# Kernel optimization log

Measured on AMD Instinct MI355X. Metric: run time of the kernel, lower is better.

The kernel has to match this reference:

```python
import jax, jax.numpy as jnp
import numpy as np
import math

Z_DIM = 1024
DOWN = 512
UP = 1024
HEADS = 16
ROPE_HD = 64
HEAD_DIM = Z_DIM // HEADS  # 64, used only in softmax scale
V_HD = UP // HEADS


def _rope(x, num_heads, head_dim, base=10000.0):
    # x: [bs, L, num_heads*head_dim] -> [bs, num_heads, L, head_dim]
    bs, L, _ = x.shape
    theta = 1.0 / (base ** (jnp.arange(0, head_dim, 2, dtype=jnp.float32) / head_dim))
    pe = jnp.arange(L, dtype=jnp.float32)[:, None] * theta[None, :]  # [L, hd/2]
    # NOTE: faithful to source, which stores sin(pos) in cos_pos and cos(pos) in sin_pos
    cos_pos = jnp.repeat(jnp.sin(pe), 2, axis=-1)  # [L, hd]
    sin_pos = jnp.repeat(jnp.cos(pe), 2, axis=-1)
    q = x.reshape(bs, L, num_heads, head_dim).transpose(0, 2, 1, 3)
    q2 = jnp.stack([-q[..., 1::2], q[..., ::2]], axis=-1).reshape(q.shape)
    return q * cos_pos + q2 * sin_pos


def setup_inputs() -> dict:
    key = jax.random.key(0)
    ks = jax.random.split(key, 20)
    B, S = 2, 2048
    s = lambda fan_in: 1.0 / math.sqrt(fan_in)
    d = {
        'query': jax.random.normal(ks[0], (B, S, Z_DIM), jnp.float32),
        'key': jax.random.normal(ks[1], (B, S, Z_DIM), jnp.float32),
        'value': jax.random.normal(ks[2], (B, S, Z_DIM), jnp.float32),
        'w_dkv': jax.random.uniform(ks[3], (Z_DIM, DOWN), jnp.float32, -s(Z_DIM), s(Z_DIM)),
        'b_dkv': jnp.zeros((DOWN,), jnp.float32),
        'w_uk': jax.random.uniform(ks[4], (DOWN, UP), jnp.float32, -s(DOWN), s(DOWN)),
        'b_uk': jnp.zeros((UP,), jnp.float32),
        'w_uv': jax.random.uniform(ks[5], (DOWN, UP), jnp.float32, -s(DOWN), s(DOWN)),
        'b_uv': jnp.zeros((UP,), jnp.float32),
        'w_dq': jax.random.uniform(ks[6], (Z_DIM, DOWN), jnp.float32, -s(Z_DIM), s(Z_DIM)),
        'b_dq': jnp.zeros((DOWN,), jnp.float32),
        'w_uq': jax.random.uniform(ks[7], (DOWN, UP), jnp.float32, -s(DOWN), s(DOWN)),
        'b_uq': jnp.zeros((UP,), jnp.float32),
        'w_qr': jax.random.uniform(ks[8], (DOWN, ROPE_HD * HEADS), jnp.float32, -s(DOWN), s(DOWN)),
        'b_qr': jnp.zeros((ROPE_HD * HEADS,), jnp.float32),
        'w_kr': jax.random.uniform(ks[9], (Z_DIM, ROPE_HD), jnp.float32, -s(Z_DIM), s(Z_DIM)),
        'b_kr': jnp.zeros((ROPE_HD,), jnp.float32),
        'w_fc': jax.random.uniform(ks[10], (HEADS * V_HD, Z_DIM), jnp.float32, -s(HEADS * V_HD), s(HEADS * V_HD)),
        'b_fc': jnp.zeros((Z_DIM,), jnp.float32),
    }
    return d


def reference(query, key, value, w_dkv, b_dkv, w_uk, b_uk, w_uv, b_uv,
              w_dq, b_dq, w_uq, b_uq, w_qr, b_qr, w_kr, b_kr, w_fc, b_fc):
    bs, S, _ = query.shape
    c_t_kv = key @ w_dkv + b_dkv                      # [B,S,down]
    k_t_c = c_t_kv @ w_uk + b_uk                      # [B,S,up]
    v_t_c = c_t_kv @ w_uv + b_uv                      # [B,S,up]
    c_t_q = query @ w_dq + b_dq                       # [B,S,down]
    q_t_c = c_t_q @ w_uq + b_uq                       # [B,S,up]
    q_t_r = _rope(c_t_q @ w_qr + b_qr, HEADS, ROPE_HD)  # [B,H,S,rope_hd]
    k_t_r = _rope(key @ w_kr + b_kr, 1, ROPE_HD)         # [B,1,S,rope_hd]

    q_t_c = q_t_c.reshape(bs, S, HEADS, V_HD).transpose(0, 2, 1, 3)  # [B,H,S,dc]
    q = jnp.concatenate([q_t_c, q_t_r], axis=-1)                      # [B,H,S,dc+dr]
    k_t_c = k_t_c.reshape(bs, S, HEADS, V_HD).transpose(0, 2, 1, 3)
    k = jnp.concatenate([k_t_c, jnp.broadcast_to(k_t_r, (bs, HEADS, S, ROPE_HD))], axis=-1)

    scores = jnp.einsum('bhqd,bhkd->bhqk', q, k)
    scale = math.sqrt(HEAD_DIM) + math.sqrt(ROPE_HD)
    attn = jax.nn.softmax(scores / scale, axis=-1)    # dropout is identity (eval / p=0)

    v = v_t_c.reshape(bs, S, HEADS, V_HD).transpose(0, 2, 1, 3)
    out = jnp.einsum('bhqk,bhkd->bhqd', attn, v)      # [B,H,S,v_hd]
    out = out.transpose(0, 2, 1, 3).reshape(bs, S, HEADS * V_HD)
    return out @ w_fc + b_fc
```

## Files before the change

kernel.cpp:

```cpp
#include <hip/hip_runtime.h>
#include <hip/hip_bf16.h>
#include <hip/hip_fp16.h>

typedef __attribute__((ext_vector_type(8))) short    bf16x8;
typedef __attribute__((ext_vector_type(4))) float    f32x4;
typedef __attribute__((ext_vector_type(4))) _Float16 f16x4;
typedef __attribute__((ext_vector_type(8))) _Float16 f16x8;
typedef __attribute__((ext_vector_type(2))) __fp16   fp16x2_raw;

typedef const void __attribute__((address_space(1))) gvoid_t;
typedef void __attribute__((address_space(3)))       lvoid_t;

static __device__ __forceinline__ void gload_lds16(const void* g, void* l) {
    __builtin_amdgcn_global_load_lds((gvoid_t*)g, (lvoid_t*)l, 16, 0, 0);
}

static __device__ __forceinline__ short bfbits(float f) {
    union { __hip_bfloat16 h; short s; } u;
    u.h = __float2bfloat16(f);
    return u.s;
}

static __device__ __forceinline__ float rope_val(float val, int col, int row, int Smask) {
    float other = __shfl_xor(val, 1);
    float theta = __expf(-0.28782313662425572f * (float)((col >> 1) & 31));
    float sp, cp;
    __sincosf((float)(row & Smask) * theta, &sp, &cp);
    return (col & 1) ? fmaf(val, sp, other * cp) : fmaf(val, sp, -other * cp);
}

struct TJob { const float* src; __hip_bfloat16* dst; int K, N, tx; };
struct PrepArgs {
    const float* query; const float* key;
    __hip_bfloat16* q_bf; __hip_bfloat16* k_bf; int n8; int cvtBlocks; int tBlocks;
    TJob j[8]; int start[8];
    const float *b_dkv, *b_kr, *b_uk, *b_uv, *b_uq, *b_qr;
    float *bcat1, *bcat2, *bcat3;
};

__global__ __launch_bounds__(256) void prep_kernel(PrepArgs A) {
    __shared__ __hip_bfloat16 tile[64][72];
    int bid = blockIdx.x;
    if (bid < A.cvtBlocks) {
        int t = bid * 256 + threadIdx.x;
        const float* src;
        __hip_bfloat16* dst;
        int i;
        if (t < A.n8) { src = A.query; dst = A.q_bf; i = t; }
        else          { src = A.key;   dst = A.k_bf; i = t - A.n8; }
        float4 a = ((const float4*)src)[2 * i];
        float4 b = ((const float4*)src)[2 * i + 1];
        bf16x8 o;
        o[0] = bfbits(a.x); o[1] = bfbits(a.y); o[2] = bfbits(a.z); o[3] = bfbits(a.w);
        o[4] = bfbits(b.x); o[5] = bfbits(b.y); o[6] = bfbits(b.z); o[7] = bfbits(b.w);
        ((bf16x8*)dst)[i] = o;
        return;
    }
    bid -= A.cvtBlocks;
    if (bid < A.tBlocks) {
        int ji = 0;
#pragma unroll
        for (int k = 1; k < 8; ++k) if (bid >= A.start[k]) ji = k;
        const TJob J = A.j[ji];
        const int local = bid - A.start[ji];
        const int kb = (local % J.tx) * 64;
        const int nb = (local / J.tx) * 64;
        const int c  = threadIdx.x & 63;
        const int r0 = threadIdx.x >> 6;
        if (nb < J.N) {
#pragma unroll
            for (int i = 0; i < 16; ++i) {
                int r = r0 + i * 4;
                tile[r][c] = __float2bfloat16(J.src[(size_t)(kb + r) * J.N + nb + c]);
            }
            __syncthreads();
#pragma unroll
            for (int i = 0; i < 16; ++i) {
                int r = r0 + i * 4;
                J.dst[(size_t)(nb + r) * J.K + kb + c] = tile[c][r];
            }
        } else {
            __hip_bfloat16 z = __float2bfloat16(0.0f);
#pragma unroll
            for (int i = 0; i < 16; ++i) {
                int r = r0 + i * 4;
                J.dst[(size_t)(nb + r) * J.K + kb + c] = z;
            }
        }
        return;
    }
    bid -= A.tBlocks;
    int t = bid * 256 + threadIdx.x;
    if (t < 640) {
        A.bcat1[t] = (t < 512) ? A.b_dkv[t] : ((t - 512) < 64 ? A.b_kr[t - 512] : 0.0f);
    } else if (t < 2688) {
        int u = t - 640;
        A.bcat2[u] = (u < 1024) ? A.b_uq[u] : A.b_qr[u - 1024];
    } else if (t < 4736) {
        int u = t - 2688;
        A.bcat3[u] = (u < 1024) ? A.b_uk[u] : A.b_uv[u - 1024];
    }
}

struct GJob {
    const __hip_bfloat16* A; const __hip_bfloat16* Bt; const float* bias;
    void* C0; void* C1; int N, K, lda, ldb, ldc; float scale; int mode;
};

__global__ __launch_bounds__(256) void gemm_dual(GJob j0, GJob j1, int split, int Smask) {
    __shared__ __align__(16) __hip_bfloat16 sA[2][64 * 32];
    __shared__ __align__(16) __hip_bfloat16 sB[2][128 * 32];
    const GJob J  = (blockIdx.x < (unsigned)split) ? j0 : j1;
    const int bx  = (blockIdx.x < (unsigned)split) ? blockIdx.x : blockIdx.x - split;
    const int tid  = threadIdx.x;
    const int wid  = tid >> 6;
    const int lane = tid & 63;
    const int lr   = lane & 15;
    const int lg   = lane >> 4;
    const int mb   = blockIdx.y * 64;
    const int nb   = bx * 128;
    const int wr   = (wid >> 1) * 32;
    const int wc   = (wid & 1) * 64;

    auto stage = [&](int bufi, int k0) {
        {
            int e   = wid * 512 + lane * 8;
            int row = e >> 5, col = e & 31;
            gload_lds16(J.A + (size_t)(mb + row) * J.lda + (k0 + col), &sA[bufi][wid * 512]);
        }
#pragma unroll
        for (int j = 0; j < 2; ++j) {
            int cb  = wid * 2 + j;
            int e   = cb * 512 + lane * 8;
            int row = e >> 5, col = e & 31;
            gload_lds16(J.Bt + (size_t)(nb + row) * J.ldb + (k0 + col), &sB[bufi][cb * 512]);
        }
    };

    f32x4 acc[2][4] = {};
    const int nt = J.K / 32;
    stage(0, 0);
    asm volatile("s_waitcnt vmcnt(0)" ::: "memory");
    __syncthreads();

    for (int t = 0; t < nt; ++t) {
        const int cur = t & 1;
        if (t + 1 < nt) stage(cur ^ 1, (t + 1) * 32);
        bf16x8 af[2], bfr[4];
#pragma unroll
        for (int m = 0; m < 2; ++m)
            af[m] = *(const bf16x8*)&sA[cur][(wr + m * 16 + lr) * 32 + lg * 8];
#pragma unroll
        for (int n = 0; n < 4; ++n)
            bfr[n] = *(const bf16x8*)&sB[cur][(wc + n * 16 + lr) * 32 + lg * 8];
#pragma unroll
        for (int m = 0; m < 2; ++m)
#pragma unroll
            for (int n = 0; n < 4; ++n)
                acc[m][n] = __builtin_amdgcn_mfma_f32_16x16x32_bf16(af[m], bfr[n], acc[m][n], 0, 0, 0);
        asm volatile("s_waitcnt vmcnt(0)" ::: "memory");
        __syncthreads();
    }

#pragma unroll
    for (int n = 0; n < 4; ++n) {
        int col  = nb + wc + n * 16 + lr;
        float bv = J.bias ? J.bias[col] : 0.0f;
        bool doRope = (J.mode == 5) && (col >= 512) && (col < 576);
#pragma unroll
        for (int m = 0; m < 2; ++m) {
#pragma unroll
            for (int r = 0; r < 4; ++r) {
                int row    = mb + wr + m * 16 + lg * 4 + r;
                float val  = (acc[m][n][r] + bv) * J.scale;
                if (doRope) val = rope_val(val, col, row, Smask);
                if (J.mode == 1) ((float*)J.C0)[(size_t)row * J.ldc + col] = val;
                else             ((__hip_bfloat16*)J.C0)[(size_t)row * J.ldc + col] = __float2bfloat16(val);
            }
        }
    }
}

__global__ __launch_bounds__(256) void gemm128_dual(GJob j0, GJob j1, int split, int Rtot) {
    __shared__ __align__(16) char smem[128 * 132 * 2];
    __hip_bfloat16* sA = (__hip_bfloat16*)smem;
    __hip_bfloat16* sB = (__hip_bfloat16*)(smem + 16384);
    const GJob J  = (blockIdx.x < (unsigned)split) ? j0 : j1;
    const int bx  = (blockIdx.x < (unsigned)split) ? blockIdx.x : blockIdx.x - split;
    const int tid  = threadIdx.x;
    const int wid  = tid >> 6;
    const int lane = tid & 63;
    const int lr   = lane & 15;
    const int lg   = lane >> 4;
    const int mb   = blockIdx.y * 128;
    const int nb   = bx * 128;
    const int wr   = (wid >> 1) * 64;
    const int wc   = (wid & 1) * 64;
    const int Smask = (Rtot >> 1) - 1;

    auto stage = [&](int bufi, int k0) {
#pragma unroll
        for (int j = 0; j < 2; ++j) {
            int c   = wid * 2 + j;
            int e   = c * 512 + lane * 8;
            int row = e >> 5, col = e & 31;
            gload_lds16(J.A + (size_t)(mb + row) * J.lda + (k0 + col), &sA[bufi * 4096 + c * 512]);
        }
#pragma unroll
        for (int j = 0; j < 2; ++j) {
            int c   = wid * 2 + j;
            int e   = c * 512 + lane * 8;
            int row = e >> 5, col = e & 31;
            gload_lds16(J.Bt + (size_t)(nb + row) * J.ldb + (k0 + col), &sB[bufi * 4096 + c * 512]);
        }
    };

    f32x4 acc[4][4] = {};
    const int nt = J.K / 32;
    stage(0, 0);
    asm volatile("s_waitcnt vmcnt(0)" ::: "memory");
    __syncthreads();

    for (int t = 0; t < nt; ++t) {
        const int cur = t & 1;
        if (t + 1 < nt) stage(cur ^ 1, (t + 1) * 32);
        bf16x8 af[4], bfr[4];
#pragma unroll
        for (int m = 0; m < 4; ++m)
            af[m] = *(const bf16x8*)&sA[cur * 4096 + (wr + m * 16 + lr) * 32 + lg * 8];
#pragma unroll
        for (int n = 0; n < 4; ++n)
            bfr[n] = *(const bf16x8*)&sB[cur * 4096 + (wc + n * 16 + lr) * 32 + lg * 8];
#pragma unroll
        for (int m = 0; m < 4; ++m)
#pragma unroll
            for (int n = 0; n < 4; ++n)
                acc[m][n] = __builtin_amdgcn_mfma_f32_16x16x32_bf16(af[m], bfr[n], acc[m][n], 0, 0, 0);
        asm volatile("s_waitcnt vmcnt(0)" ::: "memory");
        __syncthreads();
    }

    if (J.mode == 3 && nb >= 1024) {
        _Float16* T = (_Float16*)smem;
#pragma unroll
        for (int n = 0; n < 4; ++n) {
            int cl = wc + n * 16 + lr;
            float bv = J.bias[nb + cl];
#pragma unroll
            for (int m = 0; m < 4; ++m)
#pragma unroll
                for (int r = 0; r < 4; ++r)
                    T[cl * 132 + wr + m * 16 + lg * 4 + r] =
                        (_Float16)((acc[m][n][r] + bv) * J.scale);
        }
        __syncthreads();
        const int vd   = tid >> 1;
        const int half = tid & 1;
        _Float16* dst = (_Float16*)J.C1 + (size_t)(nb - 1024 + vd) * Rtot + mb + half * 64;
        const _Float16* srcT = T + vd * 132 + half * 64;
#pragma unroll
        for (int j = 0; j < 8; ++j)
            *(f16x8*)&dst[j * 8] = *(const f16x8*)&srcT[j * 8];
        return;
    }

#pragma unroll
    for (int n = 0; n < 4; ++n) {
        int col  = nb + wc + n * 16 + lr;
        float bv = J.bias ? J.bias[col] : 0.0f;
        bool doRope = (J.mode == 4) && (col >= 1024);
#pragma unroll
        for (int m = 0; m < 4; ++m) {
#pragma unroll
            for (int r = 0; r < 4; ++r) {
                int row    = mb + wr + m * 16 + lg * 4 + r;
                float val  = (acc[m][n][r] + bv) * J.scale;
                if (doRope) val = rope_val(val, col, row, Smask);
                if (J.mode == 3) ((__hip_bfloat16*)J.C0)[(size_t)row * 1024 + col] = __float2bfloat16(val);
                else             ((__hip_bfloat16*)J.C0)[(size_t)row * J.ldc + col] = __float2bfloat16(val);
            }
        }
    }
}

__global__ __launch_bounds__(512, 4) void attn_kernel(const __hip_bfloat16* __restrict__ qcat,
                                                      const __hip_bfloat16* __restrict__ ktc,
                                                      const __hip_bfloat16* __restrict__ kr,
                                                      const _Float16* __restrict__ vtcT,
                                                      __hip_bfloat16* __restrict__ outp,
                                                      int S, int R) {
    __shared__ __align__(16) char lds[2][24 * 1024];
    const int tid  = threadIdx.x;
    const int wid  = tid >> 6;
    const int lane = tid & 63;
    const int lr   = lane & 15;
    const int lg   = lane >> 4;

    const int NQ   = S / 128;
    const int L    = blockIdx.x;
    const int slot = L >> 3;
    const int gg   = (L & 7) + 8 * (slot / NQ);
    const int qt   = slot % NQ;
    const int h    = gg & 15;
    const int b    = gg >> 4;
    const size_t base = (size_t)b * S;
    const int qb   = qt * 128 + wid * 16;

    auto stage = [&](int bufi, int kt) {
        char* bufK = lds[bufi];
        char* bufV = lds[bufi] + 16 * 1024;
#pragma unroll
        for (int j = 0; j < 2; ++j) {
            int c   = wid * 2 + j;
            int rho = c * 4 + (lane >> 4);
            int u   = (lane & 15) ^ (rho & 15);
            const __hip_bfloat16* src = (u < 8)
                ? ktc + (base + kt + rho) * 1024 + h * 64 + u * 8
                : kr  + (base + kt + rho) * 640 + (u & 7) * 8;
            gload_lds16(src, bufK + c * 1024);
        }
        {
            int c   = wid;
            int rho = c * 8 + (lane >> 3);
            int u   = (lane & 7) ^ (rho & 7);
            gload_lds16(vtcT + (size_t)(h * 64 + rho) * R + base + kt + u * 8,
                        bufV + c * 1024);
        }
    };

    bf16x8 qf[4];
    {
        size_t row = base + qb + lr;
        const __hip_bfloat16* pq = qcat + row * 2048 + h * 64;
        qf[0] = *(const bf16x8*)(pq + lg * 8);
        qf[1] = *(const bf16x8*)(pq + 32 + lg * 8);
        qf[2] = *(const bf16x8*)(pq + 1024 + lg * 8);
        qf[3] = *(const bf16x8*)(pq + 1024 + 32 + lg * 8);
    }

    int kbase[4], vbase[4];
#pragma unroll
    for (int c = 0; c < 4; ++c)
        kbase[c] = lr * 256 + (((c * 4 + lg) ^ lr) << 4);
#pragma unroll
    for (int st = 0; st < 4; ++st)
        vbase[st] = lr * 128 + ((((st * 2 + (lg >> 1)) ^ (lr & 7)) << 4) + (lg & 1) * 8);

    f32x4 oacc[4] = {};
    float lrun = 0.0f;
#if __has_builtin(__builtin_amdgcn_fdot2)
    fp16x2_raw one2;
    one2[0] = (__fp16)1.0f; one2[1] = (__fp16)1.0f;
#endif

    const int NT = S / 64;
    stage(0, 0);
    __syncthreads();

    for (int t = 0; t < NT; ++t) {
        const int cur = t & 1;
        if (t + 1 < NT) stage(cur ^ 1, (t + 1) * 64);

        const char* bufK = lds[cur];
        const char* bufV = lds[cur] + 16 * 1024;

        f32x4 sacc[4] = {};
        __builtin_amdgcn_s_setprio(1);
#pragma unroll
        for (int st = 0; st < 4; ++st)
#pragma unroll
            for (int c = 0; c < 4; ++c) {
                bf16x8 kf = *(const bf16x8*)(bufK + st * 4096 + kbase[c]);
                sacc[st] = __builtin_amdgcn_mfma_f32_16x16x32_bf16(kf, qf[c], sacc[st], 0, 0, 0);
            }
        __builtin_amdgcn_s_setprio(0);

        float p[4][4];
#pragma unroll
        for (int st = 0; st < 4; ++st)
#pragma unroll
            for (int r = 0; r < 4; ++r)
                p[st][r] = __builtin_exp2f(sacc[st][r]);
        __builtin_amdgcn_s_setprio(1);
#pragma unroll
        for (int st = 0; st < 4; ++st) {
            union { fp16x2_raw h2[2]; f16x4 v; } pu;
            pu.h2[0] = __builtin_amdgcn_cvt_pkrtz(p[st][0], p[st][1]);
            pu.h2[1] = __builtin_amdgcn_cvt_pkrtz(p[st][2], p[st][3]);
#if __has_builtin(__builtin_amdgcn_fdot2)
            lrun = __builtin_amdgcn_fdot2(pu.h2[0], one2, lrun, false);
            lrun = __builtin_amdgcn_fdot2(pu.h2[1], one2, lrun, false);
#else
            lrun += p[st][0] + p[st][1] + p[st][2] + p[st][3];
#endif
#pragma unroll
            for (int vt = 0; vt < 4; ++vt) {
                f16x4 vf = *(const f16x4*)(bufV + vt * 2048 + vbase[st]);
                oacc[vt] = __builtin_amdgcn_mfma_f32_16x16x16f16(vf, pu.v, oacc[vt], 0, 0, 0);
            }
        }
        __builtin_amdgcn_s_setprio(0);
        __syncthreads();
    }

    lrun += __shfl_xor(lrun, 16);
    lrun += __shfl_xor(lrun, 32);
    float inv = 1.0f / lrun;
    size_t rowoff = (base + qb + lr) << 10;
#pragma unroll
    for (int vt = 0; vt < 4; ++vt)
#pragma unroll
        for (int r = 0; r < 4; ++r)
            outp[rowoff + h * 64 + vt * 16 + lg * 4 + r] =
                __float2bfloat16(oacc[vt][r] * inv);
}

extern "C" void kernel_launch(void* const* d_in, const int* in_sizes, int n_in,
                              void* d_out, int out_size, void* d_ws, size_t ws_size,
                              hipStream_t stream) {
    const float* query = (const float*)d_in[0];
    const float* key   = (const float*)d_in[1];
    const float* w_dkv = (const float*)d_in[3];
    const float* b_dkv = (const float*)d_in[4];
    const float* w_uk  = (const float*)d_in[5];
    const float* b_uk  = (const float*)d_in[6];
    const float* w_uv  = (const float*)d_in[7];
    const float* b_uv  = (const float*)d_in[8];
    const float* w_dq  = (const float*)d_in[9];
    const float* b_dq  = (const float*)d_in[10];
    const float* w_uq  = (const float*)d_in[11];
    const float* b_uq  = (const float*)d_in[12];
    const float* w_qr  = (const float*)d_in[13];
    const float* b_qr  = (const float*)d_in[14];
    const float* w_kr  = (const float*)d_in[15];
    const float* b_kr  = (const float*)d_in[16];
    const float* w_fc  = (const float*)d_in[17];
    const float* b_fc  = (const float*)d_in[18];

    const int B = 2;
    const int R = in_sizes[0] / 1024;
    const int S = R / B;
    const float QSCALE = 1.4426950408889634f / 16.0f;

    char* ws = (char*)d_ws;
    size_t off = 0;
    auto alloc = [&](size_t bytes) -> char* {
        char* p = ws + off;
        off += (bytes + 255) & ~(size_t)255;
        return p;
    };

    __hip_bfloat16* q_bf  = (__hip_bfloat16*)alloc((size_t)R * 1024 * 2);
    __hip_bfloat16* k_bf  = (__hip_bfloat16*)alloc((size_t)R * 1024 * 2);
    __hip_bfloat16* wcat1 = (__hip_bfloat16*)alloc(640 * 1024 * 2);
    __hip_bfloat16* wdq_t = (__hip_bfloat16*)alloc(512 * 1024 * 2);
    __hip_bfloat16* wcat3 = (__hip_bfloat16*)alloc(2048 * 512 * 2);
    __hip_bfloat16* wcat2 = (__hip_bfloat16*)alloc(2048 * 512 * 2);
    __hip_bfloat16* wfc_t = (__hip_bfloat16*)alloc(1024 * 1024 * 2);
    float*          bcat1 = (float*)alloc(640 * 4);
    float*          bcat2 = (float*)alloc(2048 * 4);
    float*          bcat3 = (float*)alloc(2048 * 4);
    __hip_bfloat16* ckkr  = (__hip_bfloat16*)alloc((size_t)R * 640 * 2);
    __hip_bfloat16* c_q   = (__hip_bfloat16*)alloc((size_t)R * 512 * 2);
    __hip_bfloat16* ktc   = (__hip_bfloat16*)alloc((size_t)R * 1024 * 2);
    _Float16*       vtcT  = (_Float16*)alloc((size_t)R * 1024 * 2);
    __hip_bfloat16* qcat  = (__hip_bfloat16*)alloc((size_t)R * 2048 * 2);
    __hip_bfloat16* attn_out = q_bf;

    PrepArgs PA;
    PA.query = query; PA.key = key; PA.q_bf = q_bf; PA.k_bf = k_bf;
    PA.n8 = R * 1024 / 8;
    PA.cvtBlocks = 2 * PA.n8 / 256;
    PA.j[0] = {w_dkv, wcat1,              1024, 512,  16};
    PA.j[1] = {w_kr,  wcat1 + 512 * 1024, 1024, 64,   16};
    PA.j[2] = {w_dq,  wdq_t,              1024, 512,  16};
    PA.j[3] = {w_uk,  wcat3,              512,  1024, 8};
    PA.j[4] = {w_uv,  wcat3 + 1024 * 512, 512,  1024, 8};
    PA.j[5] = {w_uq,  wcat2,              512,  1024, 8};
    PA.j[6] = {w_qr,  wcat2 + 1024 * 512, 512,  1024, 8};
    PA.j[7] = {w_fc,  wfc_t,              1024, 1024, 16};
    {
        int st = 0;
        const int counts[8] = {128, 32, 128, 128, 128, 128, 128, 256};
        for (int i = 0; i < 8; ++i) { PA.start[i] = st; st += counts[i]; }
        PA.tBlocks = st;
    }
    PA.b_dkv = b_dkv; PA.b_kr = b_kr; PA.b_uk = b_uk; PA.b_uv = b_uv;
    PA.b_uq = b_uq;   PA.b_qr = b_qr;
    PA.bcat1 = bcat1; PA.bcat2 = bcat2; PA.bcat3 = bcat3;
    prep_kernel<<<dim3(PA.cvtBlocks + PA.tBlocks + 19), 256, 0, stream>>>(PA);

    GJob ja0 = {k_bf, wcat1, bcat1, ckkr, nullptr, 640, 1024, 1024, 1024, 640, 1.0f, 5};
    GJob ja1 = {q_bf, wdq_t, b_dq,  c_q,  nullptr, 512, 1024, 1024, 1024, 512, 1.0f, 0};
    gemm_dual<<<dim3(9, R / 64), 256, 0, stream>>>(ja0, ja1, 5, S - 1);

    GJob jb0 = {ckkr, wcat3, bcat3, ktc,  vtcT,    2048, 512, 640, 512, 1024, 1.0f,   3};
    GJob jb1 = {c_q,  wcat2, bcat2, qcat, nullptr, 2048, 512, 512, 512, 2048, QSCALE, 4};
    gemm128_dual<<<dim3(32, R / 128), 256, 0, stream>>>(jb0, jb1, 16, R);

    attn_kernel<<<dim3((S / 128) * 16 * B), 512, 0, stream>>>(qcat, ktc, ckkr + 512, vtcT, attn_out, S, R);

    GJob jc0 = {attn_out, wfc_t, b_fc, d_out, nullptr, 1024, 1024, 1024, 1024, 1024, 1.0f, 1};
    gemm_dual<<<dim3(8, R / 64), 256, 0, stream>>>(jc0, jc0, 8, S - 1);
}
```

Measured before the change: 178.0 us.

## Unify GEMMs into one 64x128 kernel with K=64 tiles and XOR-swizzled LDS

Replaces the two GEMM kernels with a single 64x128-tile kernel that stages K in 64-wide chunks and XOR-swizzles the LDS layout to avoid bank conflicts on fragment reads. The 128x128 up-projection GEMM now runs with 64-row tiles, so it launches twice as many blocks, and the transposed-V and rope epilogues move into the shared kernel. The goal is fewer barriers per K step, fewer LDS conflicts and better occupancy, at the cost of less operand reuse per block for the large GEMM.

```diff
diff --git a/kernel.cpp b/kernel.cpp
--- a/kernel.cpp
+++ b/kernel.cpp
@@ -107,9 +107,10 @@
     void* C0; void* C1; int N, K, lda, ldb, ldc; float scale; int mode;
 };
 
-__global__ __launch_bounds__(256) void gemm_dual(GJob j0, GJob j1, int split, int Smask) {
-    __shared__ __align__(16) __hip_bfloat16 sA[2][64 * 32];
-    __shared__ __align__(16) __hip_bfloat16 sB[2][128 * 32];
+__global__ __launch_bounds__(256) void gemm64(GJob j0, GJob j1, int split, int Smask, int Rtot) {
+    __shared__ __align__(16) char smem[49152];
+    __hip_bfloat16* sA = (__hip_bfloat16*)smem;
+    __hip_bfloat16* sB = (__hip_bfloat16*)(smem + 16384);
     const GJob J  = (blockIdx.x < (unsigned)split) ? j0 : j1;
     const int bx  = (blockIdx.x < (unsigned)split) ? blockIdx.x : blockIdx.x - split;
     const int tid  = threadIdx.x;
@@ -123,50 +124,86 @@
     const int wc   = (wid & 1) * 64;
 
     auto stage = [&](int bufi, int k0) {
-        {
-            int e   = wid * 512 + lane * 8;
-            int row = e >> 5, col = e & 31;
-            gload_lds16(J.A + (size_t)(mb + row) * J.lda + (k0 + col), &sA[bufi][wid * 512]);
-        }
 #pragma unroll
         for (int j = 0; j < 2; ++j) {
-            int cb  = wid * 2 + j;
-            int e   = cb * 512 + lane * 8;
-            int row = e >> 5, col = e & 31;
-            gload_lds16(J.Bt + (size_t)(nb + row) * J.ldb + (k0 + col), &sB[bufi][cb * 512]);
+            int c   = wid * 2 + j;
+            int rho = c * 8 + (lane >> 3);
+            int u   = (lane & 7) ^ (rho & 7);
+            gload_lds16(J.A + (size_t)(mb + rho) * J.lda + (k0 + u * 8),
+                        &sA[bufi * 4096 + c * 512]);
+        }
+#pragma unroll
+        for (int j = 0; j < 4; ++j) {
+            int c   = wid * 4 + j;
+            int rho = c * 8 + (lane >> 3);
+            int u   = (lane & 7) ^ (rho & 7);
+            gload_lds16(J.Bt + (size_t)(nb + rho) * J.ldb + (k0 + u * 8),
+                        &sB[bufi * 8192 + c * 512]);
         }
     };
 
     f32x4 acc[2][4] = {};
-    const int nt = J.K / 32;
+    const int nt = J.K / 64;
     stage(0, 0);
     asm volatile("s_waitcnt vmcnt(0)" ::: "memory");
     __syncthreads();
 
     for (int t = 0; t < nt; ++t) {
         const int cur = t & 1;
-        if (t + 1 < nt) stage(cur ^ 1, (t + 1) * 32);
-        bf16x8 af[2], bfr[4];
-#pragma unroll
-        for (int m = 0; m < 2; ++m)
-            af[m] = *(const bf16x8*)&sA[cur][(wr + m * 16 + lr) * 32 + lg * 8];
-#pragma unroll
-        for (int n = 0; n < 4; ++n)
-            bfr[n] = *(const bf16x8*)&sB[cur][(wc + n * 16 + lr) * 32 + lg * 8];
-#pragma unroll
-        for (int m = 0; m < 2; ++m)
-#pragma unroll
-            for (int n = 0; n < 4; ++n)
-                acc[m][n] = __builtin_amdgcn_mfma_f32_16x16x32_bf16(af[m], bfr[n], acc[m][n], 0, 0, 0);
+        if (t + 1 < nt) stage(cur ^ 1, (t + 1) * 64);
+#pragma unroll
+        for (int kk = 0; kk < 2; ++kk) {
+            bf16x8 af[2], bfr[4];
+#pragma unroll
+            for (int m = 0; m < 2; ++m) {
+                int row = wr + m * 16 + lr;
+                af[m] = *(const bf16x8*)&sA[cur * 4096 + row * 64 + (((kk * 4 + lg) ^ (row & 7)) << 3)];
+            }
+#pragma unroll
+            for (int n = 0; n < 4; ++n) {
+                int row = wc + n * 16 + lr;
+                bfr[n] = *(const bf16x8*)&sB[cur * 8192 + row * 64 + (((kk * 4 + lg) ^ (row & 7)) << 3)];
+            }
+#pragma unroll
+            for (int m = 0; m < 2; ++m)
+#pragma unroll
+                for (int n = 0; n < 4; ++n)
+                    acc[m][n] = __builtin_amdgcn_mfma_f32_16x16x32_bf16(af[m], bfr[n], acc[m][n], 0, 0, 0);
+        }
         asm volatile("s_waitcnt vmcnt(0)" ::: "memory");
         __syncthreads();
+    }
+
+    if (J.mode == 3 && nb >= 1024) {
+        _Float16* T = (_Float16*)smem;
+#pragma unroll
+        for (int n = 0; n < 4; ++n) {
+            int cl = wc + n * 16 + lr;
+            float bv = J.bias[nb + cl];
+#pragma unroll
+            for (int m = 0; m < 2; ++m)
+#pragma unroll
+                for (int r = 0; r < 4; ++r)
+                    T[cl * 72 + wr + m * 16 + lg * 4 + r] =
+                        (_Float16)((acc[m][n][r] + bv) * J.scale);
+        }
+        __syncthreads();
+        const int vd   = tid >> 1;
+        const int half = tid & 1;
+        _Float16* dst = (_Float16*)J.C1 + (size_t)(nb - 1024 + vd) * Rtot + mb + half * 32;
+        const _Float16* srcT = T + vd * 72 + half * 32;
+#pragma unroll
+        for (int j = 0; j < 4; ++j)
+            *(f16x8*)&dst[j * 8] = *(const f16x8*)&srcT[j * 8];
+        return;
     }
 
 #pragma unroll
     for (int n = 0; n < 4; ++n) {
         int col  = nb + wc + n * 16 + lr;
         float bv = J.bias ? J.bias[col] : 0.0f;
-        bool doRope = (J.mode == 5) && (col >= 512) && (col < 576);
+        bool doRope = (J.mode == 4 && col >= 1024) ||
+                      (J.mode == 5 && col >= 512 && col < 576);
 #pragma unroll
         for (int m = 0; m < 2; ++m) {
 #pragma unroll
@@ -174,110 +211,9 @@
                 int row    = mb + wr + m * 16 + lg * 4 + r;
                 float val  = (acc[m][n][r] + bv) * J.scale;
                 if (doRope) val = rope_val(val, col, row, Smask);
-                if (J.mode == 1) ((float*)J.C0)[(size_t)row * J.ldc + col] = val;
-                else             ((__hip_bfloat16*)J.C0)[(size_t)row * J.ldc + col] = __float2bfloat16(val);
-            }
-        }
-    }
-}
-
-__global__ __launch_bounds__(256) void gemm128_dual(GJob j0, GJob j1, int split, int Rtot) {
-    __shared__ __align__(16) char smem[128 * 132 * 2];
-    __hip_bfloat16* sA = (__hip_bfloat16*)smem;
-    __hip_bfloat16* sB = (__hip_bfloat16*)(smem + 16384);
-    const GJob J  = (blockIdx.x < (unsigned)split) ? j0 : j1;
-    const int bx  = (blockIdx.x < (unsigned)split) ? blockIdx.x : blockIdx.x - split;
-    const int tid  = threadIdx.x;
-    const int wid  = tid >> 6;
-    const int lane = tid & 63;
-    const int lr   = lane & 15;
-    const int lg   = lane >> 4;
-    const int mb   = blockIdx.y * 128;
-    const int nb   = bx * 128;
-    const int wr   = (wid >> 1) * 64;
-    const int wc   = (wid & 1) * 64;
-    const int Smask = (Rtot >> 1) - 1;
-
-    auto stage = [&](int bufi, int k0) {
-#pragma unroll
-        for (int j = 0; j < 2; ++j) {
-            int c   = wid * 2 + j;
-            int e   = c * 512 + lane * 8;
-            int row = e >> 5, col = e & 31;
-            gload_lds16(J.A + (size_t)(mb + row) * J.lda + (k0 + col), &sA[bufi * 4096 + c * 512]);
-        }
-#pragma unroll
-        for (int j = 0; j < 2; ++j) {
-            int c   = wid * 2 + j;
-            int e   = c * 512 + lane * 8;
-            int row = e >> 5, col = e & 31;
-            gload_lds16(J.Bt + (size_t)(nb + row) * J.ldb + (k0 + col), &sB[bufi * 4096 + c * 512]);
-        }
-    };
-
-    f32x4 acc[4][4] = {};
-    const int nt = J.K / 32;
-    stage(0, 0);
-    asm volatile("s_waitcnt vmcnt(0)" ::: "memory");
-    __syncthreads();
-
-    for (int t = 0; t < nt; ++t) {
-        const int cur = t & 1;
-        if (t + 1 < nt) stage(cur ^ 1, (t + 1) * 32);
-        bf16x8 af[4], bfr[4];
-#pragma unroll
-        for (int m = 0; m < 4; ++m)
-            af[m] = *(const bf16x8*)&sA[cur * 4096 + (wr + m * 16 + lr) * 32 + lg * 8];
-#pragma unroll
-        for (int n = 0; n < 4; ++n)
-            bfr[n] = *(const bf16x8*)&sB[cur * 4096 + (wc + n * 16 + lr) * 32 + lg * 8];
-#pragma unroll
-        for (int m = 0; m < 4; ++m)
-#pragma unroll
-            for (int n = 0; n < 4; ++n)
-                acc[m][n] = __builtin_amdgcn_mfma_f32_16x16x32_bf16(af[m], bfr[n], acc[m][n], 0, 0, 0);
-        asm volatile("s_waitcnt vmcnt(0)" ::: "memory");
-        __syncthreads();
-    }
-
-    if (J.mode == 3 && nb >= 1024) {
-        _Float16* T = (_Float16*)smem;
-#pragma unroll
-        for (int n = 0; n < 4; ++n) {
-            int cl = wc + n * 16 + lr;
-            float bv = J.bias[nb + cl];
-#pragma unroll
-            for (int m = 0; m < 4; ++m)
-#pragma unroll
-                for (int r = 0; r < 4; ++r)
-                    T[cl * 132 + wr + m * 16 + lg * 4 + r] =
-                        (_Float16)((acc[m][n][r] + bv) * J.scale);
-        }
-        __syncthreads();
-        const int vd   = tid >> 1;
-        const int half = tid & 1;
-        _Float16* dst = (_Float16*)J.C1 + (size_t)(nb - 1024 + vd) * Rtot + mb + half * 64;
-        const _Float16* srcT = T + vd * 132 + half * 64;
-#pragma unroll
-        for (int j = 0; j < 8; ++j)
-            *(f16x8*)&dst[j * 8] = *(const f16x8*)&srcT[j * 8];
-        return;
-    }
-
-#pragma unroll
-    for (int n = 0; n < 4; ++n) {
-        int col  = nb + wc + n * 16 + lr;
-        float bv = J.bias ? J.bias[col] : 0.0f;
-        bool doRope = (J.mode == 4) && (col >= 1024);
-#pragma unroll
-        for (int m = 0; m < 4; ++m) {
-#pragma unroll
-            for (int r = 0; r < 4; ++r) {
-                int row    = mb + wr + m * 16 + lg * 4 + r;
-                float val  = (acc[m][n][r] + bv) * J.scale;
-                if (doRope) val = rope_val(val, col, row, Smask);
-                if (J.mode == 3) ((__hip_bfloat16*)J.C0)[(size_t)row * 1024 + col] = __float2bfloat16(val);
-                else             ((__hip_bfloat16*)J.C0)[(size_t)row * J.ldc + col] = __float2bfloat16(val);
+                if (J.mode == 1)      ((float*)J.C0)[(size_t)row * J.ldc + col] = val;
+                else if (J.mode == 3) ((__hip_bfloat16*)J.C0)[(size_t)row * 1024 + col] = __float2bfloat16(val);
+                else                  ((__hip_bfloat16*)J.C0)[(size_t)row * J.ldc + col] = __float2bfloat16(val);
             }
         }
     }
@@ -492,14 +428,14 @@
 
     GJob ja0 = {k_bf, wcat1, bcat1, ckkr, nullptr, 640, 1024, 1024, 1024, 640, 1.0f, 5};
     GJob ja1 = {q_bf, wdq_t, b_dq,  c_q,  nullptr, 512, 1024, 1024, 1024, 512, 1.0f, 0};
-    gemm_dual<<<dim3(9, R / 64), 256, 0, stream>>>(ja0, ja1, 5, S - 1);
+    gemm64<<<dim3(9, R / 64), 256, 0, stream>>>(ja0, ja1, 5, S - 1, R);
 
     GJob jb0 = {ckkr, wcat3, bcat3, ktc,  vtcT,    2048, 512, 640, 512, 1024, 1.0f,   3};
     GJob jb1 = {c_q,  wcat2, bcat2, qcat, nullptr, 2048, 512, 512, 512, 2048, QSCALE, 4};
-    gemm128_dual<<<dim3(32, R / 128), 256, 0, stream>>>(jb0, jb1, 16, R);
+    gemm64<<<dim3(32, R / 64), 256, 0, stream>>>(jb0, jb1, 16, S - 1, R);
 
     attn_kernel<<<dim3((S / 128) * 16 * B), 512, 0, stream>>>(qcat, ktc, ckkr + 512, vtcT, attn_out, S, R);
 
     GJob jc0 = {attn_out, wfc_t, b_fc, d_out, nullptr, 1024, 1024, 1024, 1024, 1024, 1.0f, 1};
-    gemm_dual<<<dim3(8, R / 64), 256, 0, stream>>>(jc0, jc0, 8, S - 1);
-}
+    gemm64<<<dim3(8, R / 64), 256, 0, stream>>>(jc0, jc0, 8, S - 1, R);
+}
```

Result: no change. 177.1 us (median of 2 runs) (-0.5%).
